# Optimization experiments

Measured on AMD Instinct MI355X. Metric: run time of the kernel, lower is better.

Reference implementation:

```python
import jax, jax.numpy as jnp
import numpy as np

N_NODES = 100000


def gcn_conv(x, edge_index, edge_weight, W, b):
    # PyG GCNConv: x' = D^{-1/2} (A + I) D^{-1/2} (x W) + b
    n = x.shape[0]
    h = x @ W  # [N, out]
    src, dst = edge_index[0], edge_index[1]
    loop = jnp.arange(n, dtype=edge_index.dtype)
    src2 = jnp.concatenate([src, loop])
    dst2 = jnp.concatenate([dst, loop])
    ew2 = jnp.concatenate([edge_weight, jnp.ones((n,), dtype=x.dtype)])
    deg = jax.ops.segment_sum(ew2, dst2, num_segments=n)  # weighted in-degree incl self-loop
    dinv = jnp.where(deg > 0, jax.lax.rsqrt(deg), 0.0)
    norm = dinv[src2] * ew2 * dinv[dst2]  # [E+N]
    msgs = h[src2] * norm[:, None]  # gather + scale
    out = jax.ops.segment_sum(msgs, dst2, num_segments=n)  # scatter-add at targets
    return out + b


def setup_inputs() -> dict:
    key = jax.random.key(0)
    k1, k2, k3, k4, k5 = jax.random.split(key, 5)
    F_in, H, C = 128, 64, 16
    E = 1600000
    x = jax.random.normal(k1, (N_NODES, F_in), dtype=jnp.float32)
    edge_index = jax.random.randint(k2, (2, E), 0, N_NODES, dtype=jnp.int64)
    edge_weights = jax.random.uniform(k3, (E,), dtype=jnp.float32)
    W1 = jax.random.normal(k4, (F_in, H), dtype=jnp.float32) * (1.0 / np.sqrt(F_in))
    b1 = jnp.zeros((H,), dtype=jnp.float32)
    W2 = jax.random.normal(k5, (H, C), dtype=jnp.float32) * (1.0 / np.sqrt(H))
    b2 = jnp.zeros((C,), dtype=jnp.float32)
    return {"x": x, "edge_index": edge_index, "edge_weights": edge_weights,
            "W1": W1, "b1": b1, "W2": W2, "b2": b2}


def reference(x, edge_index, edge_weights, W1, b1, W2, b2):
    h = gcn_conv(x, edge_index, edge_weights, W1, b1)
    h = jax.nn.relu(h)
    # dropout inactive at inference (F.dropout with training=False is identity)
    h = gcn_conv(h, edge_index, edge_weights, W2, b2)
    return jax.nn.log_softmax(h, axis=1)
```

## Files before the change

kernel.cpp:

```cpp
#include <hip/hip_runtime.h>


#define BSHIFT 7
#define BNODES 128
#define NBUK_MAX 1024
#define CSTR 16
#define CAP 3072
#define CHUNK 4096
#define EPB 16

typedef unsigned short ushort_t;
typedef unsigned int uint_t;

__device__ inline ushort_t f2bf(float f) {
    uint_t u = __float_as_uint(f);
    return (ushort_t)((u + 0x7FFF + ((u >> 16) & 1)) >> 16);
}
__device__ inline float bf2f(ushort_t b) {
    return __uint_as_float(((uint_t)b) << 16);
}

__global__ __launch_bounds__(1024) void k_binit(int* __restrict__ bcur, int nbuk) {
    int t = threadIdx.x;
    if (t < nbuk) bcur[t * CSTR] = t * CAP;
}

__global__ __launch_bounds__(256) void k_p1(const int* __restrict__ src,
                                            const int* __restrict__ dst,
                                            const float* __restrict__ ew,
                                            int* __restrict__ bcur,
                                            int2* __restrict__ tmp, int E, int nbuk) {
    __shared__ int lcnt[NBUK_MAX];
    __shared__ int lbase[NBUK_MAX];
    const int t = threadIdx.x;
    const int base = blockIdx.x * CHUNK;
    for (int j = t; j < nbuk; j += 256) lcnt[j] = 0;
    __syncthreads();
    int d_r[EPB];
#pragma unroll
    for (int k = 0; k < EPB; ++k) {
        int e = base + k * 256 + t;
        int d = (e < E) ? dst[e] : -1;
        d_r[k] = d;
        if (d >= 0) atomicAdd(&lcnt[d >> BSHIFT], 1);
    }
    __syncthreads();
    for (int j = t; j < nbuk; j += 256) {
        int c = lcnt[j];
        lbase[j] = c ? atomicAdd(&bcur[j * CSTR], c) : 0;
        lcnt[j] = 0;
    }
    __syncthreads();
#pragma unroll
    for (int k = 0; k < EPB; ++k) {
        int d = d_r[k];
        if (d < 0) continue;
        int e = base + k * 256 + t;
        int b = d >> BSHIFT;
        int p = lbase[b] + atomicAdd(&lcnt[b], 1);
        if (p >= nbuk * CAP) continue;
        int2 pk;
        pk.x = src[e] | ((d & (BNODES - 1)) << 17);
        pk.y = __float_as_int(ew[e]);
        tmp[p] = pk;
    }
}

__global__ __launch_bounds__(1024) void k_pscan(const int* __restrict__ bcur,
                                                int* __restrict__ boff, int nbuk) {
    __shared__ int lds[1024];
    const int t = threadIdx.x;
    int v = (t < nbuk) ? (bcur[t * CSTR] - t * CAP) : 0;
    lds[t] = v;
    __syncthreads();
    for (int off = 1; off < 1024; off <<= 1) {
        int u = (t >= off) ? lds[t - off] : 0;
        __syncthreads();
        lds[t] += u;
        __syncthreads();
    }
    if (t < nbuk) boff[t] = lds[t] - v;
    if (t == nbuk - 1) boff[nbuk] = lds[t];
}

__global__ __launch_bounds__(256) void k_p2(const int2* __restrict__ tmp,
                                            const int* __restrict__ bcur,
                                            const int* __restrict__ boff,
                                            int* __restrict__ rowptr,
                                            int2* __restrict__ epack,
                                            float* __restrict__ dinv,
                                            int n, int nbuk) {
    __shared__ int cnt[BNODES];
    __shared__ int pos[BNODES];
    __shared__ float degf[BNODES];
    const int b = blockIdx.x, t = threadIdx.x;
    const int node0 = b << BSHIFT;
    if (t < BNODES) { cnt[t] = 0; degf[t] = 0.f; }
    __syncthreads();
    const int lo_t = b * CAP, hi_t = bcur[b * CSTR];
    const int outb = boff[b];
    for (int i = lo_t + t; i < hi_t; i += 256) {
        int2 pk = tmp[i];
        int dlo = (pk.x >> 17) & (BNODES - 1);
        atomicAdd(&cnt[dlo], 1);
        atomicAdd(&degf[dlo], __int_as_float(pk.y));
    }
    __syncthreads();
    int own = (t < BNODES) ? cnt[t] : 0;
    if (t < BNODES) pos[t] = own;
    __syncthreads();
    for (int off = 1; off < BNODES; off <<= 1) {
        int u = (t < BNODES && t >= off) ? pos[t - off] : 0;
        __syncthreads();
        if (t < BNODES) pos[t] += u;
        __syncthreads();
    }
    if (t < BNODES) {
        int excl = pos[t] - own;
        int node = node0 + t;
        if (node < n) {
            rowptr[node] = outb + excl;
            dinv[node] = rsqrtf(1.0f + degf[t]);
        }
        pos[t] = excl;
    }
    if (b == nbuk - 1 && t == 0) rowptr[n] = outb + (hi_t - lo_t);
    __syncthreads();
    for (int i = lo_t + t; i < hi_t; i += 256) {
        int2 pk = tmp[i];
        int dlo = (pk.x >> 17) & (BNODES - 1);
        int p = outb + atomicAdd(&pos[dlo], 1);
        int2 o;
        o.x = pk.x & 0x1FFFF;
        o.y = pk.y;
        epack[p] = o;
    }
}

__global__ __launch_bounds__(256) void k_gemm1(const float* __restrict__ x,
                                               const float* __restrict__ W,
                                               const float* __restrict__ dinv,
                                               ushort_t* __restrict__ h, int n) {
    __shared__ float Ws[128 * 64];
    __shared__ float xs[16][128];
    const int t = threadIdx.x;
    for (int i = t; i < 128 * 64; i += 256) Ws[i] = W[i];
    const int node0 = blockIdx.x * 16;
    for (int i = t; i < 16 * 128; i += 256) {
        int nn = i >> 7, kk = i & 127;
        int node = node0 + nn;
        xs[nn][kk] = (node < n) ? x[(size_t)node * 128 + kk] : 0.0f;
    }
    __syncthreads();
    const int fg = t & 15;
    const int ng = t >> 4;
    const float4* Ws4 = (const float4*)Ws;
    float4 acc = {0.f, 0.f, 0.f, 0.f};
#pragma unroll 8
    for (int k = 0; k < 128; ++k) {
        float4 w = Ws4[k * 16 + fg];
        float xv = xs[ng][k];
        acc.x = fmaf(xv, w.x, acc.x);
        acc.y = fmaf(xv, w.y, acc.y);
        acc.z = fmaf(xv, w.z, acc.z);
        acc.w = fmaf(xv, w.w, acc.w);
    }
    const int node = node0 + ng;
    if (node < n) {
        float di = dinv[node];
        ushort_t* p = h + (size_t)node * 64 + fg * 4;
        p[0] = f2bf(acc.x * di);
        p[1] = f2bf(acc.y * di);
        p[2] = f2bf(acc.z * di);
        p[3] = f2bf(acc.w * di);
    }
}

__global__ __launch_bounds__(256) void k_agg64(const ushort_t* __restrict__ h,
                                               const int* __restrict__ rowptr,
                                               const int2* __restrict__ ep,
                                               const float* __restrict__ dinv,
                                               float* __restrict__ agg, int n) {
    const int node = (blockIdx.x * 256 + threadIdx.x) >> 6;
    const int lane = threadIdx.x & 63;
    if (node >= n) return;
    const float di = dinv[node];
    float accE = 0.f;
    const int lo = rowptr[node], hi = rowptr[node + 1];
    int i = lo;
    for (; i + 7 < hi; i += 8) {
        int2 p0 = ep[i], p1 = ep[i + 1], p2 = ep[i + 2], p3 = ep[i + 3];
        int2 p4 = ep[i + 4], p5 = ep[i + 5], p6 = ep[i + 6], p7 = ep[i + 7];
        float v0 = bf2f(h[(size_t)p0.x * 64 + lane]);
        float v1 = bf2f(h[(size_t)p1.x * 64 + lane]);
        float v2 = bf2f(h[(size_t)p2.x * 64 + lane]);
        float v3 = bf2f(h[(size_t)p3.x * 64 + lane]);
        float v4 = bf2f(h[(size_t)p4.x * 64 + lane]);
        float v5 = bf2f(h[(size_t)p5.x * 64 + lane]);
        float v6 = bf2f(h[(size_t)p6.x * 64 + lane]);
        float v7 = bf2f(h[(size_t)p7.x * 64 + lane]);
        accE = fmaf(v0, __int_as_float(p0.y), accE);
        accE = fmaf(v1, __int_as_float(p1.y), accE);
        accE = fmaf(v2, __int_as_float(p2.y), accE);
        accE = fmaf(v3, __int_as_float(p3.y), accE);
        accE = fmaf(v4, __int_as_float(p4.y), accE);
        accE = fmaf(v5, __int_as_float(p5.y), accE);
        accE = fmaf(v6, __int_as_float(p6.y), accE);
        accE = fmaf(v7, __int_as_float(p7.y), accE);
    }
    for (; i < hi; ++i) {
        int2 p = ep[i];
        accE = fmaf(bf2f(h[(size_t)p.x * 64 + lane]), __int_as_float(p.y), accE);
    }
    float self = bf2f(h[(size_t)node * 64 + lane]);
    agg[(size_t)node * 64 + lane] = di * (accE + self);
}

__global__ __launch_bounds__(256) void k_agg16(const ushort_t* __restrict__ h,
                                               const int* __restrict__ rowptr,
                                               const int2* __restrict__ ep,
                                               const float* __restrict__ dinv,
                                               float* __restrict__ agg, int n) {
    const int node = (blockIdx.x * 256 + threadIdx.x) >> 4;
    const int lane = threadIdx.x & 15;
    if (node >= n) return;
    const float di = dinv[node];
    float accE = 0.f;
    const int lo = rowptr[node], hi = rowptr[node + 1];
    int i = lo;
    for (; i + 3 < hi; i += 4) {
        int2 p0 = ep[i], p1 = ep[i + 1], p2 = ep[i + 2], p3 = ep[i + 3];
        float v0 = bf2f(h[(size_t)p0.x * 16 + lane]);
        float v1 = bf2f(h[(size_t)p1.x * 16 + lane]);
        float v2 = bf2f(h[(size_t)p2.x * 16 + lane]);
        float v3 = bf2f(h[(size_t)p3.x * 16 + lane]);
        accE = fmaf(v0, __int_as_float(p0.y), accE);
        accE = fmaf(v1, __int_as_float(p1.y), accE);
        accE = fmaf(v2, __int_as_float(p2.y), accE);
        accE = fmaf(v3, __int_as_float(p3.y), accE);
    }
    for (; i < hi; ++i) {
        int2 p = ep[i];
        accE = fmaf(bf2f(h[(size_t)p.x * 16 + lane]), __int_as_float(p.y), accE);
    }
    float self = bf2f(h[(size_t)node * 16 + lane]);
    agg[(size_t)node * 16 + lane] = di * (accE + self);
}

__global__ __launch_bounds__(256) void k_gemm2(const float* __restrict__ a,
                                               const float* __restrict__ W,
                                               const float* __restrict__ b1,
                                               const float* __restrict__ dinv,
                                               ushort_t* __restrict__ h2, int n) {
    __shared__ float Ws[64 * 16];
    __shared__ float xs[32][68];
    const int t = threadIdx.x;
    for (int i = t; i < 64 * 16; i += 256) Ws[i] = W[i];
    const int node0 = blockIdx.x * 32;
    for (int i = t; i < 32 * 64; i += 256) {
        int nn = i >> 6, kk = i & 63;
        int node = node0 + nn;
        xs[nn][kk] = (node < n) ? fmaxf(a[(size_t)node * 64 + kk] + b1[kk], 0.0f) : 0.0f;
    }
    __syncthreads();
    const int f = t & 15;
    const int ng = t >> 4;
    float a0 = 0.f, a1 = 0.f;
#pragma unroll 4
    for (int k = 0; k < 64; ++k) {
        float wv = Ws[k * 16 + f];
        a0 = fmaf(xs[ng][k], wv, a0);
        a1 = fmaf(xs[ng + 16][k], wv, a1);
    }
    if (node0 + ng < n)
        h2[(size_t)(node0 + ng) * 16 + f] = f2bf(a0 * dinv[node0 + ng]);
    if (node0 + ng + 16 < n)
        h2[(size_t)(node0 + ng + 16) * 16 + f] = f2bf(a1 * dinv[node0 + ng + 16]);
}

__global__ void k_logsoftmax(float* __restrict__ out, const float* __restrict__ b2, int n) {
    int i = blockIdx.x * blockDim.x + threadIdx.x;
    if (i >= n) return;
    const size_t base = (size_t)i * 16;
    float v[16];
#pragma unroll
    for (int f = 0; f < 16; ++f) v[f] = out[base + f] + b2[f];
    float m = v[0];
#pragma unroll
    for (int f = 1; f < 16; ++f) m = fmaxf(m, v[f]);
    float s = 0.f;
#pragma unroll
    for (int f = 0; f < 16; ++f) s += __expf(v[f] - m);
    float lse = __logf(s);
#pragma unroll
    for (int f = 0; f < 16; ++f) out[base + f] = v[f] - m - lse;
}

extern "C" void kernel_launch(void* const* d_in, const int* in_sizes, int n_in,
                              void* d_out, int out_size, void* d_ws, size_t ws_size,
                              hipStream_t stream) {
    const float* x  = (const float*)d_in[0];
    const int*   ei = (const int*)d_in[1];
    const float* ew = (const float*)d_in[2];
    const float* W1 = (const float*)d_in[3];
    const float* b1 = (const float*)d_in[4];
    const float* W2 = (const float*)d_in[5];
    const float* b2 = (const float*)d_in[6];
    float* out = (float*)d_out;

    const int n = in_sizes[0] / 128;
    const int E = in_sizes[2];
    const int* srcv = ei;
    const int* dstv = ei + E;
    const int nbuk = (n + BNODES - 1) >> BSHIFT;

    float* wsf = (float*)d_ws;
    size_t off = 0;
    float* dinv = wsf + off; off += n;
    ushort_t* h1b = (ushort_t*)(wsf + off); off += (size_t)n * 32;
    float* agg1 = wsf + off; off += (size_t)n * 64;
    off = (off + 1) & ~(size_t)1;
    int2* epack = (int2*)(wsf + off); off += (size_t)E * 2;
    int* rowptr = (int*)(wsf + off); off += n + 1;
    int* boff_d = (int*)(wsf + off); off += NBUK_MAX + 1;
    int* bcur   = (int*)(wsf + off); off += (size_t)NBUK_MAX * CSTR;
    int2* tmp   = (int2*)agg1;

    const int TB = 256;

    k_binit<<<1, 1024, 0, stream>>>(bcur, nbuk);
    k_p1<<<(E + CHUNK - 1) / CHUNK, TB, 0, stream>>>(srcv, dstv, ew, bcur, tmp, E, nbuk);
    k_pscan<<<1, 1024, 0, stream>>>(bcur, boff_d, nbuk);
    k_p2<<<nbuk, TB, 0, stream>>>(tmp, bcur, boff_d, rowptr, epack, dinv, n, nbuk);

    k_gemm1<<<(n + 15) / 16, TB, 0, stream>>>(x, W1, dinv, h1b, n);
    k_agg64<<<(n * 64 + TB - 1) / TB, TB, 0, stream>>>(h1b, rowptr, epack, dinv, agg1, n);

    k_gemm2<<<(n + 31) / 32, TB, 0, stream>>>(agg1, W2, b1, dinv, h1b, n);
    k_agg16<<<(n * 16 + TB - 1) / TB, TB, 0, stream>>>(h1b, rowptr, epack, dinv, out, n);

    k_logsoftmax<<<(n + TB - 1) / TB, TB, 0, stream>>>(out, b2, n);
}
```

Measured before the change: 333.2 us.

## Split layer-1 features into XCD-mapped slices for L2-local gathers

```diff
diff --git a/kernel.cpp b/kernel.cpp
--- a/kernel.cpp
+++ b/kernel.cpp
@@ -11,6 +11,7 @@
 
 typedef unsigned short ushort_t;
 typedef unsigned int uint_t;
+typedef unsigned short us4 __attribute__((ext_vector_type(4)));
 
 __device__ inline ushort_t f2bf(float f) {
     uint_t u = __float_as_uint(f);
@@ -168,37 +169,48 @@
     const int node = node0 + ng;
     if (node < n) {
         float di = dinv[node];
-        ushort_t* p = h + (size_t)node * 64 + fg * 4;
-        p[0] = f2bf(acc.x * di);
-        p[1] = f2bf(acc.y * di);
-        p[2] = f2bf(acc.z * di);
-        p[3] = f2bf(acc.w * di);
-    }
-}
-
-__global__ __launch_bounds__(256) void k_agg64(const ushort_t* __restrict__ h,
-                                               const int* __restrict__ rowptr,
-                                               const int2* __restrict__ ep,
-                                               const float* __restrict__ dinv,
-                                               float* __restrict__ agg, int n) {
-    const int node = (blockIdx.x * 256 + threadIdx.x) >> 6;
-    const int lane = threadIdx.x & 63;
+        const int slice = fg >> 2;
+        size_t base = (size_t)slice * ((size_t)n * 16) + (size_t)node * 16 + (size_t)(fg & 3) * 4;
+        us4 pk;
+        pk.x = f2bf(acc.x * di);
+        pk.y = f2bf(acc.y * di);
+        pk.z = f2bf(acc.z * di);
+        pk.w = f2bf(acc.w * di);
+        *(us4*)(h + base) = pk;
+    }
+}
+
+__global__ __launch_bounds__(256) void k_agg64s(const ushort_t* __restrict__ h,
+                                                const int* __restrict__ rowptr,
+                                                const int2* __restrict__ ep,
+                                                const float* __restrict__ dinv,
+                                                float* __restrict__ agg, int n) {
+    const int bid = blockIdx.x;
+    const int xcd = bid & 7;
+    const int slice = xcd & 3;
+    const int g = ((bid >> 3) << 1) + (xcd >> 2);
+    if (g * 16 >= n) return;
+    const int t = threadIdx.x;
+    const int sub = t >> 4;
+    const int lane = t & 15;
+    const int node = g * 16 + sub;
     if (node >= n) return;
+    const ushort_t* __restrict__ hs = h + (size_t)slice * ((size_t)n * 16);
     const float di = dinv[node];
+    const int lo = rowptr[node], hi = rowptr[node + 1];
     float accE = 0.f;
-    const int lo = rowptr[node], hi = rowptr[node + 1];
     int i = lo;
     for (; i + 7 < hi; i += 8) {
         int2 p0 = ep[i], p1 = ep[i + 1], p2 = ep[i + 2], p3 = ep[i + 3];
         int2 p4 = ep[i + 4], p5 = ep[i + 5], p6 = ep[i + 6], p7 = ep[i + 7];
-        float v0 = bf2f(h[(size_t)p0.x * 64 + lane]);
-        float v1 = bf2f(h[(size_t)p1.x * 64 + lane]);
-        float v2 = bf2f(h[(size_t)p2.x * 64 + lane]);
-        float v3 = bf2f(h[(size_t)p3.x * 64 + lane]);
-        float v4 = bf2f(h[(size_t)p4.x * 64 + lane]);
-        float v5 = bf2f(h[(size_t)p5.x * 64 + lane]);
-        float v6 = bf2f(h[(size_t)p6.x * 64 + lane]);
-        float v7 = bf2f(h[(size_t)p7.x * 64 + lane]);
+        float v0 = bf2f(hs[(size_t)p0.x * 16 + lane]);
+        float v1 = bf2f(hs[(size_t)p1.x * 16 + lane]);
+        float v2 = bf2f(hs[(size_t)p2.x * 16 + lane]);
+        float v3 = bf2f(hs[(size_t)p3.x * 16 + lane]);
+        float v4 = bf2f(hs[(size_t)p4.x * 16 + lane]);
+        float v5 = bf2f(hs[(size_t)p5.x * 16 + lane]);
+        float v6 = bf2f(hs[(size_t)p6.x * 16 + lane]);
+        float v7 = bf2f(hs[(size_t)p7.x * 16 + lane]);
         accE = fmaf(v0, __int_as_float(p0.y), accE);
         accE = fmaf(v1, __int_as_float(p1.y), accE);
         accE = fmaf(v2, __int_as_float(p2.y), accE);
@@ -210,10 +222,10 @@
     }
     for (; i < hi; ++i) {
         int2 p = ep[i];
-        accE = fmaf(bf2f(h[(size_t)p.x * 64 + lane]), __int_as_float(p.y), accE);
-    }
-    float self = bf2f(h[(size_t)node * 64 + lane]);
-    agg[(size_t)node * 64 + lane] = di * (accE + self);
+        accE = fmaf(bf2f(hs[(size_t)p.x * 16 + lane]), __int_as_float(p.y), accE);
+    }
+    float self = bf2f(hs[(size_t)node * 16 + lane]);
+    agg[(size_t)node * 64 + (size_t)slice * 16 + lane] = di * (accE + self);
 }
 
 __global__ __launch_bounds__(256) void k_agg16(const ushort_t* __restrict__ h,
@@ -334,7 +346,11 @@
     k_p2<<<nbuk, TB, 0, stream>>>(tmp, bcur, boff_d, rowptr, epack, dinv, n, nbuk);
 
     k_gemm1<<<(n + 15) / 16, TB, 0, stream>>>(x, W1, dinv, h1b, n);
-    k_agg64<<<(n * 64 + TB - 1) / TB, TB, 0, stream>>>(h1b, rowptr, epack, dinv, agg1, n);
+    {
+        const int gps = (n + 15) / 16;
+        const int pairs = (gps + 1) / 2;
+        k_agg64s<<<pairs * 8, TB, 0, stream>>>(h1b, rowptr, epack, dinv, agg1, n);
+    }
 
     k_gemm2<<<(n + 31) / 32, TB, 0, stream>>>(agg1, W2, b1, dinv, h1b, n);
     k_agg16<<<(n * 16 + TB - 1) / TB, TB, 0, stream>>>(h1b, rowptr, epack, dinv, out, n);
```

Result: slower. 349.8 us (+5.0%).
